# Optimization experiments

Hardware: AMD Instinct MI355X
Metric: run time of the kernel (lower is better)

The kernel has to match this reference:

```python
import jax, jax.numpy as jnp
import numpy as np

EPS = 1e-12  # F.normalize clamp_min eps

def _l2norm(v, axis):
    return v / jnp.maximum(jnp.linalg.norm(v, axis=axis, keepdims=True), EPS)

def setup_inputs() -> dict:
    key = jax.random.key(0)
    k1, k2, k3, k4 = jax.random.split(key, 4)
    N, C, H, W, K = 256, 128, 31, 31, 64
    x = jax.random.normal(k1, (N, C, H, W), dtype=jnp.float32)
    conv_w = jax.random.normal(k2, (K, C), dtype=jnp.float32) * 0.1   # 1x1 conv weight, no bias (vladv2=False)
    centroids = jax.random.uniform(k3, (K, C), dtype=jnp.float32)     # torch.rand init
    atten_w = jax.random.normal(k4, (C,), dtype=jnp.float32) * 0.1    # attention 1x1 conv weight
    atten_b = jnp.zeros((1,), dtype=jnp.float32)
    return {"x": x, "conv_w": conv_w, "centroids": centroids, "atten_w": atten_w, "atten_b": atten_b}

def reference(x, conv_w, centroids, atten_w, atten_b):
    N, C, H, W = x.shape
    S = H * W  # 961
    # attention head: ReLU -> Conv2d(C,1,1) -> ReLU
    hmp = jax.nn.relu(jnp.einsum('nchw,c->nhw', jax.nn.relu(x), atten_w) + atten_b[0])
    hmp_f = hmp.reshape(N, S)                     # [N,S]
    # normalize input over channel dim
    xn = _l2norm(x, axis=1)
    x_f = xn.reshape(N, C, S)                     # [N,C,S]
    x_mul = x_f * hmp_f[:, None, :]               # [N,C,S] (hmp applied once)
    # soft assignment: 1x1 conv (no bias) on xn*hmp, softmax over clusters
    soft_assign = jax.nn.softmax(jnp.einsum('kc,ncs->nks', conv_w, x_mul), axis=1)
    # fused weighted residual aggregation (hmp applied a second time, as in source)
    w = soft_assign * hmp_f[:, None, :]           # [N,K,S]
    vlad = jnp.einsum('nks,ncs->nkc', w, x_mul) - centroids[None, :, :] * jnp.sum(w, axis=-1)[:, :, None]
    vlad = _l2norm(vlad, axis=2)                  # intra-normalize per cluster
    vlad = vlad.reshape(N, -1)
    vlad = _l2norm(vlad, axis=1)
    vlad = _l2norm(vlad, axis=1)                  # source normalizes flattened vlad twice
    return vlad
```

## Files before the change

kernel.cpp:

```cpp
#include <hip/hip_runtime.h>
#include <hip/hip_bf16.h>

#define N_ 256
#define C_ 128
#define S_ 961
#define K_ 64
#define TS 64
#define NTILE_LOC 8
#define NTHREADS 512

typedef __attribute__((ext_vector_type(4))) float f32x4;
typedef __attribute__((ext_vector_type(8))) _Float16 f16x8;
typedef __attribute__((ext_vector_type(4))) _Float16 f16x4;

#define MFMAF(a, b, c) __builtin_amdgcn_mfma_f32_16x16x32_f16((a), (b), (c), 0, 0, 0)

template <bool ATOMIC>
__global__ __launch_bounds__(NTHREADS, 2) void vlad_main(
    const float* __restrict__ x,
    const float* __restrict__ conv_w,
    const float* __restrict__ cent,
    const float* __restrict__ aw,
    const float* __restrict__ ab,
    float* __restrict__ out,
    float* __restrict__ ws)
{
    __shared__ _Float16 s_xs[2][C_][72];
    __shared__ _Float16 s_xT[TS][136];
    __shared__ _Float16 s_u[K_][72];
    __shared__ float s_ared[2][8][68];
    __shared__ float s_cs[8][68];
    __shared__ float s_wp[8][4][8];
    __shared__ float s_wsum[K_];

    const int tid = threadIdx.x;
    const int bid = blockIdx.x;
    const int n = bid >> 1, h = bid & 1;
    const int sbase = h * (NTILE_LOC * TS);
    const int lane = tid & 63;
    const int w = tid >> 6;
    const int la = lane & 15;
    const int lg = lane >> 4;
    const float bias = ab[0];
    const float* xn = x + (size_t)n * (C_ * S_);

    const int cb = tid >> 4;
    const int c0 = cb * 4;
    const int s0l = (tid & 15) * 4;

    float awr[4];
    #pragma unroll
    for (int r = 0; r < 4; ++r) awr[r] = aw[c0 + r];

    const int nt1 = w & 3;
    const int mtb = (w >> 2) * 2;
    const int sc = 16 * nt1 + la;
    f16x8 cw[2][4];
    #pragma unroll
    for (int m2 = 0; m2 < 2; ++m2) {
        const float* p = conv_w + (la + 16 * (mtb + m2)) * C_ + 8 * lg;
        #pragma unroll
        for (int cc = 0; cc < 4; ++cc)
            #pragma unroll
            for (int i = 0; i < 8; ++i)
                cw[m2][cc][i] = (_Float16)p[32 * cc + i];
    }

    const int mtb2 = (w & 1) * 2;
    const int ctb2 = (w >> 1) * 2;
    f32x4 acc2[2][2];
    #pragma unroll
    for (int m = 0; m < 2; ++m)
        #pragma unroll
        for (int ci = 0; ci < 2; ++ci) acc2[m][ci] = (f32x4){0.f, 0.f, 0.f, 0.f};

    float wp0[4] = {0.f, 0.f, 0.f, 0.f};
    float wp1[4] = {0.f, 0.f, 0.f, 0.f};
    float pxA[4][4], pxB[4][4];

    #pragma unroll
    for (int r = 0; r < 4; ++r) {
        const float* pr = xn + (size_t)(c0 + r) * S_ + sbase + s0l;
        pxA[r][0] = pr[0]; pxA[r][1] = pr[1]; pxA[r][2] = pr[2]; pxA[r][3] = pr[3];
    }

#define GEMM2_STEP(SB)                                                          \
    {                                                                           \
        _Pragma("unroll") for (int sc2 = 0; sc2 < 2; ++sc2) {                   \
            f16x8 ua[2];                                                        \
            _Pragma("unroll") for (int m = 0; m < 2; ++m)                       \
                ua[m] = *(const f16x8*)&s_u[la + 16*(mtb2+m)][8*lg + 32*sc2];   \
            _Pragma("unroll") for (int ci = 0; ci < 2; ++ci) {                  \
                f16x8 xb = *(const f16x8*)&s_xs[SB][la + 16*(ctb2+ci)][8*lg + 32*sc2]; \
                _Pragma("unroll") for (int m = 0; m < 2; ++m)                   \
                    acc2[m][ci] = MFMAF(ua[m], xb, acc2[m][ci]);                \
            }                                                                   \
        }                                                                       \
    }

#define TILE_BODY(T, PXC, PXN, BUF)                                             \
{                                                                               \
                                                          \
    if ((T) + 1 < NTILE_LOC) {                                                  \
        int gs = sbase + ((T)+1)*TS + s0l;                                      \
        _Pragma("unroll") for (int r = 0; r < 4; ++r) {                         \
            const float* pr = xn + (size_t)(c0+r)*S_ + gs;                      \
            if (gs + 3 < S_) {                                                  \
                PXN[r][0]=pr[0]; PXN[r][1]=pr[1]; PXN[r][2]=pr[2]; PXN[r][3]=pr[3]; \
            } else {                                                            \
                _Pragma("unroll") for (int j = 0; j < 4; ++j)                   \
                    PXN[r][j] = (gs + j < S_) ? pr[j] : 0.f;                    \
            }                                                                   \
        }                                                                       \
    }                                                                           \
                                         \
    if ((T) > 0) GEMM2_STEP((BUF)^1)                                            \
                                                   \
    {                                                                           \
        float ssqp[4], hdp[4];                                                  \
        _Pragma("unroll") for (int j = 0; j < 4; ++j) { ssqp[j]=0.f; hdp[j]=0.f; } \
        _Pragma("unroll") for (int r = 0; r < 4; ++r) {                         \
            f16x4 v;                                                            \
            _Pragma("unroll") for (int j = 0; j < 4; ++j) {                     \
                float f = PXC[r][j];                                            \
                v[j] = (_Float16)f;                                             \
                ssqp[j] += f*f;                                                 \
                hdp[j]  += fmaxf(f, 0.f)*awr[r];                                \
            }                                                                   \
            *(f16x4*)&s_xs[BUF][c0+r][s0l] = v;                                 \
        }                                                                       \
        _Pragma("unroll") for (int j = 0; j < 4; ++j) {                         \
            int srow = s0l + j;                                                 \
            int cidx = c0 ^ (((srow >> 3) & 3) << 3);                           \
            f16x4 vT = {(_Float16)PXC[0][j], (_Float16)PXC[1][j],               \
                        (_Float16)PXC[2][j], (_Float16)PXC[3][j]};              \
            *(f16x4*)&s_xT[srow][cidx] = vT;                                    \
        }                                                                       \
        _Pragma("unroll") for (int j = 0; j < 4; ++j) {                         \
            ssqp[j] += __shfl_xor(ssqp[j], 16);                                 \
            ssqp[j] += __shfl_xor(ssqp[j], 32);                                 \
            hdp[j]  += __shfl_xor(hdp[j], 16);                                  \
            hdp[j]  += __shfl_xor(hdp[j], 32);                                  \
        }                                                                       \
        if (lg == 0) {                                                          \
            f32x4 a = {ssqp[0],ssqp[1],ssqp[2],ssqp[3]};                        \
            f32x4 b = {hdp[0],hdp[1],hdp[2],hdp[3]};                            \
            *(f32x4*)&s_ared[0][w][s0l] = a;                                    \
            *(f32x4*)&s_ared[1][w][s0l] = b;                                    \
        }                                                                       \
    }                                                                           \
    __syncthreads();                                                     \
             \
    float e0[4], e1[4], hm, al, csw;                                            \
    {                                                                           \
        int srow = sc;                                                          \
        int swz = ((srow >> 3) & 3) << 3;                                       \
        f32x4 d0 = {0.f,0.f,0.f,0.f}, d1 = {0.f,0.f,0.f,0.f};                   \
        _Pragma("unroll") for (int cc = 0; cc < 4; ++cc) {                      \
            f16x8 b = *(const f16x8*)&s_xT[srow][(8*lg + 32*cc) ^ swz];         \
            d0 = MFMAF(cw[0][cc], b, d0);                                       \
            d1 = MFMAF(cw[1][cc], b, d1);                                       \
        }                                                                       \
        float ssq = s_ared[0][2*lg][sc] + s_ared[0][2*lg+1][sc];                \
        float hd  = s_ared[1][2*lg][sc] + s_ared[1][2*lg+1][sc];                \
        ssq += __shfl_xor(ssq, 16); ssq += __shfl_xor(ssq, 32);                 \
        hd  += __shfl_xor(hd, 16);  hd  += __shfl_xor(hd, 32);                  \
        int sg = sbase + (T)*TS + sc;                                           \
        hm = (sg < S_) ? fmaxf(hd + bias, 0.f) : 0.f;                           \
        al = hm / fmaxf(sqrtf(ssq), 1e-12f);                                    \
        float cs = 0.f;                                                         \
        _Pragma("unroll") for (int i = 0; i < 4; ++i) {                         \
            e0[i] = __expf(d0[i] * al);                                         \
            e1[i] = __expf(d1[i] * al);                                         \
            cs += e0[i] + e1[i];                                                \
        }                                                                       \
        cs += __shfl_xor(cs, 16); cs += __shfl_xor(cs, 32);                     \
        csw = cs;                                                               \
        if (lg == 0) s_cs[w][sc] = cs;                                          \
    }                                                                           \
    __syncthreads();                                                     \
                                                  \
    {                                                                           \
        float cst = csw + s_cs[w ^ 4][sc];                                      \
        float wl = hm * __builtin_amdgcn_rcpf(cst);                             \
        _Pragma("unroll") for (int i = 0; i < 4; ++i) {                         \
            float wv0 = e0[i] * wl;                                             \
            float wv1 = e1[i] * wl;                                             \
            wp0[i] += wv0;                                                      \
            wp1[i] += wv1;                                                      \
            s_u[16*mtb + 4*lg + i][sc]     = (_Float16)(wv0 * al);              \
            s_u[16*(mtb+1) + 4*lg + i][sc] = (_Float16)(wv1 * al);              \
        }                                                                       \
    }                                                                           \
    __syncthreads();                                                     \
}

    for (int tp = 0; tp < NTILE_LOC; tp += 2) {
        TILE_BODY(tp,     pxA, pxB, 0)
        TILE_BODY(tp + 1, pxB, pxA, 1)
    }
    GEMM2_STEP(1)

    {
        #pragma unroll
        for (int i = 0; i < 4; ++i) {
            #pragma unroll
            for (int m = 1; m < 16; m <<= 1) {
                wp0[i] += __shfl_xor(wp0[i], m);
                wp1[i] += __shfl_xor(wp1[i], m);
            }
        }
        if (la == 0) {
            #pragma unroll
            for (int i = 0; i < 4; ++i) {
                s_wp[w][lg][i]     = wp0[i];
                s_wp[w][lg][4 + i] = wp1[i];
            }
        }
    }
    __syncthreads();
    if (tid < K_) {
        int k = tid;
        int kh = k >> 5, m2 = (k >> 4) & 1, lgk = (k >> 2) & 3, ik = k & 3;
        float v = 0.f;
        #pragma unroll
        for (int q = 0; q < 4; ++q) v += s_wp[4 * kh + q][lgk][4 * m2 + ik];
        s_wsum[k] = v;
    }
    __syncthreads();

    {
        float* dst = ATOMIC ? out : (h ? ws : out);
        #pragma unroll
        for (int m = 0; m < 2; ++m) {
            #pragma unroll
            for (int ci = 0; ci < 2; ++ci) {
                int c = la + 16 * (ctb2 + ci);
                #pragma unroll
                for (int i = 0; i < 4; ++i) {
                    int k = 16 * (mtb2 + m) + 4 * lg + i;
                    float val = acc2[m][ci][i] - cent[k * C_ + c] * s_wsum[k];
                    size_t off = (size_t)n * (K_ * C_) + k * C_ + c;
                    if (ATOMIC) atomicAdd(&dst[off], val);
                    else dst[off] = val;
                }
            }
        }
    }
}

template <bool WS>
__global__ __launch_bounds__(256) void vlad_norm(
    float* __restrict__ out, const float* __restrict__ ws)
{
    __shared__ float s_rs[K_], s_f[K_];
    __shared__ float s_fin;
    const int n = blockIdx.x, tid = threadIdx.x;
    const int k = tid >> 2, q = tid & 3;
    float* po = out + (size_t)n * (K_ * C_) + k * C_ + q * 32;
    const float* pw = ws + (size_t)n * (K_ * C_) + k * C_ + q * 32;

    float v[32];
    float ssq = 0.f;
    #pragma unroll
    for (int i = 0; i < 8; ++i) {
        f32x4 a = *(const f32x4*)&po[4 * i];
        if (WS) {
            f32x4 b = *(const f32x4*)&pw[4 * i];
            a[0]+=b[0]; a[1]+=b[1]; a[2]+=b[2]; a[3]+=b[3];
        }
        #pragma unroll
        for (int j = 0; j < 4; ++j) { v[4*i+j] = a[j]; ssq += a[j]*a[j]; }
    }
    ssq += __shfl_xor(ssq, 1);
    ssq += __shfl_xor(ssq, 2);
    if (q == 0) {
        float rs = 1.0f / fmaxf(sqrtf(ssq), 1e-12f);
        s_rs[k] = rs;
        s_f[k] = ssq * rs * rs;
    }
    __syncthreads();
    if (tid < 64) {
        float f = s_f[tid];
        #pragma unroll
        for (int m = 1; m < 64; m <<= 1) f += __shfl_xor(f, m);
        if (tid == 0) {
            float n1 = sqrtf(f);
            float sc1 = 1.0f / fmaxf(n1, 1e-12f);
            float n2 = n1 * sc1;
            float sc2 = 1.0f / fmaxf(n2, 1e-12f);
            s_fin = sc1 * sc2;
        }
    }
    __syncthreads();
    float sc = s_rs[k] * s_fin;
    #pragma unroll
    for (int i = 0; i < 8; ++i) {
        f32x4 a = {v[4*i]*sc, v[4*i+1]*sc, v[4*i+2]*sc, v[4*i+3]*sc};
        *(f32x4*)&po[4 * i] = a;
    }
}

extern "C" void kernel_launch(void* const* d_in, const int* in_sizes, int n_in,
                              void* d_out, int out_size, void* d_ws, size_t ws_size,
                              hipStream_t stream) {
    const float* x      = (const float*)d_in[0];
    const float* conv_w = (const float*)d_in[1];
    const float* cent   = (const float*)d_in[2];
    const float* aw     = (const float*)d_in[3];
    const float* ab     = (const float*)d_in[4];
    float* outp = (float*)d_out;
    float* wsp  = (float*)d_ws;

    const size_t need = (size_t)N_ * K_ * C_ * sizeof(float);
    if (ws_size >= need) {
        vlad_main<false><<<2 * N_, NTHREADS, 0, stream>>>(x, conv_w, cent, aw, ab, outp, wsp);
        vlad_norm<true><<<N_, 256, 0, stream>>>(outp, wsp);
    } else {
        hipMemsetAsync(d_out, 0, need, stream);
        vlad_main<true><<<2 * N_, NTHREADS, 0, stream>>>(x, conv_w, cent, aw, ab, outp, wsp);
        vlad_norm<false><<<N_, 256, 0, stream>>>(outp, nullptr);
    }
}
```

Measured before the change: 61.68 us.

## Drop software pipelining and move conv weights to LDS to raise occupancy

Removes the register prefetch of the next x tile and the double-buffered s_xs, runs GEMM2 inline after each tile behind an extra barrier, and stages conv_w fragments in shared memory instead of registers. Launch bounds go from 2 to 8 blocks per CU, trading per-block latency hiding for more resident waves. This adds a fourth __syncthreads per tile and extra LDS reads of conv_w every tile. Global loads are no longer overlapped with compute within a block.

```diff
diff --git a/kernel.cpp b/kernel.cpp
--- a/kernel.cpp
+++ b/kernel.cpp
@@ -16,7 +16,7 @@
 #define MFMAF(a, b, c) __builtin_amdgcn_mfma_f32_16x16x32_f16((a), (b), (c), 0, 0, 0)
 
 template <bool ATOMIC>
-__global__ __launch_bounds__(NTHREADS, 2) void vlad_main(
+__global__ __launch_bounds__(NTHREADS, 8) void vlad_main(
     const float* __restrict__ x,
     const float* __restrict__ conv_w,
     const float* __restrict__ cent,
@@ -25,8 +25,9 @@
     float* __restrict__ out,
     float* __restrict__ ws)
 {
-    __shared__ _Float16 s_xs[2][C_][72];
+    __shared__ _Float16 s_xs[C_][72];
     __shared__ _Float16 s_xT[TS][136];
+    __shared__ _Float16 s_cw[16][64][8];
     __shared__ _Float16 s_u[K_][72];
     __shared__ float s_ared[2][8][68];
     __shared__ float s_cs[8][68];
@@ -52,19 +53,23 @@
     #pragma unroll
     for (int r = 0; r < 4; ++r) awr[r] = aw[c0 + r];
 
+    {
+        int b = tid >> 5;
+        int mt = b >> 2, cc = b & 3;
+        #pragma unroll
+        for (int dl = 0; dl < 2; ++dl) {
+            int l = (tid & 31) * 2 + dl;
+            const float* p = conv_w + ((l & 15) + 16 * mt) * C_ + 8 * (l >> 4) + 32 * cc;
+            f16x8 v;
+            #pragma unroll
+            for (int i = 0; i < 8; ++i) v[i] = (_Float16)p[i];
+            *(f16x8*)&s_cw[b][l][0] = v;
+        }
+    }
+
     const int nt1 = w & 3;
     const int mtb = (w >> 2) * 2;
     const int sc = 16 * nt1 + la;
-    f16x8 cw[2][4];
-    #pragma unroll
-    for (int m2 = 0; m2 < 2; ++m2) {
-        const float* p = conv_w + (la + 16 * (mtb + m2)) * C_ + 8 * lg;
-        #pragma unroll
-        for (int cc = 0; cc < 4; ++cc)
-            #pragma unroll
-            for (int i = 0; i < 8; ++i)
-                cw[m2][cc][i] = (_Float16)p[32 * cc + i];
-    }
 
     const int mtb2 = (w & 1) * 2;
     const int ctb2 = (w >> 1) * 2;
@@ -76,130 +81,123 @@
 
     float wp0[4] = {0.f, 0.f, 0.f, 0.f};
     float wp1[4] = {0.f, 0.f, 0.f, 0.f};
-    float pxA[4][4], pxB[4][4];
-
-    #pragma unroll
-    for (int r = 0; r < 4; ++r) {
-        const float* pr = xn + (size_t)(c0 + r) * S_ + sbase + s0l;
-        pxA[r][0] = pr[0]; pxA[r][1] = pr[1]; pxA[r][2] = pr[2]; pxA[r][3] = pr[3];
-    }
-
-#define GEMM2_STEP(SB)                                                          \
-    {                                                                           \
-        _Pragma("unroll") for (int sc2 = 0; sc2 < 2; ++sc2) {                   \
-            f16x8 ua[2];                                                        \
-            _Pragma("unroll") for (int m = 0; m < 2; ++m)                       \
-                ua[m] = *(const f16x8*)&s_u[la + 16*(mtb2+m)][8*lg + 32*sc2];   \
-            _Pragma("unroll") for (int ci = 0; ci < 2; ++ci) {                  \
-                f16x8 xb = *(const f16x8*)&s_xs[SB][la + 16*(ctb2+ci)][8*lg + 32*sc2]; \
-                _Pragma("unroll") for (int m = 0; m < 2; ++m)                   \
-                    acc2[m][ci] = MFMAF(ua[m], xb, acc2[m][ci]);                \
-            }                                                                   \
-        }                                                                       \
-    }
-
-#define TILE_BODY(T, PXC, PXN, BUF)                                             \
-{                                                                               \
-                                                          \
-    if ((T) + 1 < NTILE_LOC) {                                                  \
-        int gs = sbase + ((T)+1)*TS + s0l;                                      \
-        _Pragma("unroll") for (int r = 0; r < 4; ++r) {                         \
-            const float* pr = xn + (size_t)(c0+r)*S_ + gs;                      \
-            if (gs + 3 < S_) {                                                  \
-                PXN[r][0]=pr[0]; PXN[r][1]=pr[1]; PXN[r][2]=pr[2]; PXN[r][3]=pr[3]; \
-            } else {                                                            \
-                _Pragma("unroll") for (int j = 0; j < 4; ++j)                   \
-                    PXN[r][j] = (gs + j < S_) ? pr[j] : 0.f;                    \
-            }                                                                   \
-        }                                                                       \
-    }                                                                           \
-                                         \
-    if ((T) > 0) GEMM2_STEP((BUF)^1)                                            \
-                                                   \
-    {                                                                           \
-        float ssqp[4], hdp[4];                                                  \
-        _Pragma("unroll") for (int j = 0; j < 4; ++j) { ssqp[j]=0.f; hdp[j]=0.f; } \
-        _Pragma("unroll") for (int r = 0; r < 4; ++r) {                         \
-            f16x4 v;                                                            \
-            _Pragma("unroll") for (int j = 0; j < 4; ++j) {                     \
-                float f = PXC[r][j];                                            \
-                v[j] = (_Float16)f;                                             \
-                ssqp[j] += f*f;                                                 \
-                hdp[j]  += fmaxf(f, 0.f)*awr[r];                                \
-            }                                                                   \
-            *(f16x4*)&s_xs[BUF][c0+r][s0l] = v;                                 \
-        }                                                                       \
-        _Pragma("unroll") for (int j = 0; j < 4; ++j) {                         \
-            int srow = s0l + j;                                                 \
-            int cidx = c0 ^ (((srow >> 3) & 3) << 3);                           \
-            f16x4 vT = {(_Float16)PXC[0][j], (_Float16)PXC[1][j],               \
-                        (_Float16)PXC[2][j], (_Float16)PXC[3][j]};              \
-            *(f16x4*)&s_xT[srow][cidx] = vT;                                    \
-        }                                                                       \
-        _Pragma("unroll") for (int j = 0; j < 4; ++j) {                         \
-            ssqp[j] += __shfl_xor(ssqp[j], 16);                                 \
-            ssqp[j] += __shfl_xor(ssqp[j], 32);                                 \
-            hdp[j]  += __shfl_xor(hdp[j], 16);                                  \
-            hdp[j]  += __shfl_xor(hdp[j], 32);                                  \
-        }                                                                       \
-        if (lg == 0) {                                                          \
-            f32x4 a = {ssqp[0],ssqp[1],ssqp[2],ssqp[3]};                        \
-            f32x4 b = {hdp[0],hdp[1],hdp[2],hdp[3]};                            \
-            *(f32x4*)&s_ared[0][w][s0l] = a;                                    \
-            *(f32x4*)&s_ared[1][w][s0l] = b;                                    \
-        }                                                                       \
-    }                                                                           \
-    __syncthreads();                                                     \
-             \
-    float e0[4], e1[4], hm, al, csw;                                            \
-    {                                                                           \
-        int srow = sc;                                                          \
-        int swz = ((srow >> 3) & 3) << 3;                                       \
-        f32x4 d0 = {0.f,0.f,0.f,0.f}, d1 = {0.f,0.f,0.f,0.f};                   \
-        _Pragma("unroll") for (int cc = 0; cc < 4; ++cc) {                      \
-            f16x8 b = *(const f16x8*)&s_xT[srow][(8*lg + 32*cc) ^ swz];         \
-            d0 = MFMAF(cw[0][cc], b, d0);                                       \
-            d1 = MFMAF(cw[1][cc], b, d1);                                       \
-        }                                                                       \
-        float ssq = s_ared[0][2*lg][sc] + s_ared[0][2*lg+1][sc];                \
-        float hd  = s_ared[1][2*lg][sc] + s_ared[1][2*lg+1][sc];                \
-        ssq += __shfl_xor(ssq, 16); ssq += __shfl_xor(ssq, 32);                 \
-        hd  += __shfl_xor(hd, 16);  hd  += __shfl_xor(hd, 32);                  \
-        int sg = sbase + (T)*TS + sc;                                           \
-        hm = (sg < S_) ? fmaxf(hd + bias, 0.f) : 0.f;                           \
-        al = hm / fmaxf(sqrtf(ssq), 1e-12f);                                    \
-        float cs = 0.f;                                                         \
-        _Pragma("unroll") for (int i = 0; i < 4; ++i) {                         \
-            e0[i] = __expf(d0[i] * al);                                         \
-            e1[i] = __expf(d1[i] * al);                                         \
-            cs += e0[i] + e1[i];                                                \
-        }                                                                       \
-        cs += __shfl_xor(cs, 16); cs += __shfl_xor(cs, 32);                     \
-        csw = cs;                                                               \
-        if (lg == 0) s_cs[w][sc] = cs;                                          \
-    }                                                                           \
-    __syncthreads();                                                     \
-                                                  \
-    {                                                                           \
-        float cst = csw + s_cs[w ^ 4][sc];                                      \
-        float wl = hm * __builtin_amdgcn_rcpf(cst);                             \
-        _Pragma("unroll") for (int i = 0; i < 4; ++i) {                         \
-            float wv0 = e0[i] * wl;                                             \
-            float wv1 = e1[i] * wl;                                             \
-            wp0[i] += wv0;                                                      \
-            wp1[i] += wv1;                                                      \
-            s_u[16*mtb + 4*lg + i][sc]     = (_Float16)(wv0 * al);              \
-            s_u[16*(mtb+1) + 4*lg + i][sc] = (_Float16)(wv1 * al);              \
-        }                                                                       \
-    }                                                                           \
-    __syncthreads();                                                     \
-}
-
-    for (int tp = 0; tp < NTILE_LOC; tp += 2) {
-        TILE_BODY(tp,     pxA, pxB, 0)
-        TILE_BODY(tp + 1, pxB, pxA, 1)
-    }
-    GEMM2_STEP(1)
+
+    for (int T = 0; T < NTILE_LOC; ++T) {
+        {
+            int gs = sbase + T * TS + s0l;
+            f16x4 hv[4];
+            float ssqp[4] = {0.f, 0.f, 0.f, 0.f};
+            float hdp[4]  = {0.f, 0.f, 0.f, 0.f};
+            #pragma unroll
+            for (int r = 0; r < 4; ++r) {
+                const float* pr = xn + (size_t)(c0 + r) * S_ + gs;
+                float f0, f1, f2, f3;
+                if (gs + 3 < S_) {
+                    f0 = pr[0]; f1 = pr[1]; f2 = pr[2]; f3 = pr[3];
+                } else {
+                    f0 = (gs + 0 < S_) ? pr[0] : 0.f;
+                    f1 = (gs + 1 < S_) ? pr[1] : 0.f;
+                    f2 = (gs + 2 < S_) ? pr[2] : 0.f;
+                    f3 = (gs + 3 < S_) ? pr[3] : 0.f;
+                }
+                f16x4 v = {(_Float16)f0, (_Float16)f1, (_Float16)f2, (_Float16)f3};
+                hv[r] = v;
+                ssqp[0] += f0 * f0; ssqp[1] += f1 * f1;
+                ssqp[2] += f2 * f2; ssqp[3] += f3 * f3;
+                hdp[0] += fmaxf(f0, 0.f) * awr[r];
+                hdp[1] += fmaxf(f1, 0.f) * awr[r];
+                hdp[2] += fmaxf(f2, 0.f) * awr[r];
+                hdp[3] += fmaxf(f3, 0.f) * awr[r];
+                *(f16x4*)&s_xs[c0 + r][s0l] = v;
+            }
+            #pragma unroll
+            for (int j = 0; j < 4; ++j) {
+                int srow = s0l + j;
+                int cidx = c0 ^ (((srow >> 3) & 3) << 3);
+                f16x4 vT = {hv[0][j], hv[1][j], hv[2][j], hv[3][j]};
+                *(f16x4*)&s_xT[srow][cidx] = vT;
+            }
+            #pragma unroll
+            for (int j = 0; j < 4; ++j) {
+                ssqp[j] += __shfl_xor(ssqp[j], 16);
+                ssqp[j] += __shfl_xor(ssqp[j], 32);
+                hdp[j]  += __shfl_xor(hdp[j], 16);
+                hdp[j]  += __shfl_xor(hdp[j], 32);
+            }
+            if (lg == 0) {
+                f32x4 a = {ssqp[0], ssqp[1], ssqp[2], ssqp[3]};
+                f32x4 b = {hdp[0], hdp[1], hdp[2], hdp[3]};
+                *(f32x4*)&s_ared[0][w][s0l] = a;
+                *(f32x4*)&s_ared[1][w][s0l] = b;
+            }
+        }
+        __syncthreads();
+
+        float e0[4], e1[4], hm, al, csw;
+        {
+            int swz = ((sc >> 3) & 3) << 3;
+            f32x4 d0 = {0.f, 0.f, 0.f, 0.f}, d1 = {0.f, 0.f, 0.f, 0.f};
+            #pragma unroll
+            for (int cc = 0; cc < 4; ++cc) {
+                f16x8 a0 = *(const f16x8*)&s_cw[(mtb + 0) * 4 + cc][lane][0];
+                f16x8 a1 = *(const f16x8*)&s_cw[(mtb + 1) * 4 + cc][lane][0];
+                f16x8 b  = *(const f16x8*)&s_xT[sc][(8 * lg + 32 * cc) ^ swz];
+                d0 = MFMAF(a0, b, d0);
+                d1 = MFMAF(a1, b, d1);
+            }
+            float ssq = s_ared[0][2 * lg][sc] + s_ared[0][2 * lg + 1][sc];
+            float hd  = s_ared[1][2 * lg][sc] + s_ared[1][2 * lg + 1][sc];
+            ssq += __shfl_xor(ssq, 16); ssq += __shfl_xor(ssq, 32);
+            hd  += __shfl_xor(hd, 16);  hd  += __shfl_xor(hd, 32);
+            int sg = sbase + T * TS + sc;
+            hm = (sg < S_) ? fmaxf(hd + bias, 0.f) : 0.f;
+            al = hm / fmaxf(sqrtf(ssq), 1e-12f);
+            float cs = 0.f;
+            #pragma unroll
+            for (int i = 0; i < 4; ++i) {
+                e0[i] = __expf(d0[i] * al);
+                e1[i] = __expf(d1[i] * al);
+                cs += e0[i] + e1[i];
+            }
+            cs += __shfl_xor(cs, 16); cs += __shfl_xor(cs, 32);
+            csw = cs;
+            if (lg == 0) s_cs[w][sc] = cs;
+        }
+        __syncthreads();
+
+        {
+            float cst = csw + s_cs[w ^ 4][sc];
+            float wl = hm * __builtin_amdgcn_rcpf(cst);
+            #pragma unroll
+            for (int i = 0; i < 4; ++i) {
+                float wv0 = e0[i] * wl;
+                float wv1 = e1[i] * wl;
+                wp0[i] += wv0;
+                wp1[i] += wv1;
+                s_u[16 * mtb + 4 * lg + i][sc]       = (_Float16)(wv0 * al);
+                s_u[16 * (mtb + 1) + 4 * lg + i][sc] = (_Float16)(wv1 * al);
+            }
+        }
+        __syncthreads();
+
+        {
+            #pragma unroll
+            for (int sc2 = 0; sc2 < 2; ++sc2) {
+                f16x8 ua[2];
+                #pragma unroll
+                for (int m = 0; m < 2; ++m)
+                    ua[m] = *(const f16x8*)&s_u[la + 16 * (mtb2 + m)][8 * lg + 32 * sc2];
+                #pragma unroll
+                for (int ci = 0; ci < 2; ++ci) {
+                    f16x8 xb = *(const f16x8*)&s_xs[la + 16 * (ctb2 + ci)][8 * lg + 32 * sc2];
+                    #pragma unroll
+                    for (int m = 0; m < 2; ++m)
+                        acc2[m][ci] = MFMAF(ua[m], xb, acc2[m][ci]);
+                }
+            }
+        }
+        __syncthreads();
+    }
 
     {
         #pragma unroll
```

After: 55.86 us. 1.1x faster.
